# Optimization experiments

Hardware: AMD Instinct MI355X
Metric: run time of the kernel (lower is better)

The kernel has to match this reference:

```python
import jax, jax.numpy as jnp
import numpy as np

B, W, NN, EPG = 8, 16, 64, 1024   # batch, window, nodes/graph, trace-edges/graph
N = B * W * NN                     # 8192 flattened nodes
E = B * W * EPG                    # 131072 node-graph edges == trace rows
E2 = 4 * E                         # 524288 edge-graph (line-graph) edges
D_NODE = 128; D_LOG = 128; D_EDGE = 128
D_IN = D_NODE + D_LOG              # 256 = GATv2 node2node in_channels
H = 4
EPS = 1e-16                        # PyG softmax epsilon


def _lin(key, fan_in, fan_out):
    return jax.random.normal(key, (fan_in, fan_out), jnp.float32) * (1.0 / np.sqrt(fan_in))


def setup_inputs() -> dict:
    key = jax.random.key(0)
    ks = jax.random.split(key, 16)
    return {
        "x_node": jax.random.normal(ks[0], (B, W, NN, D_NODE), jnp.float32),
        "x_trace": jax.random.normal(ks[1], (B, W, EPG, D_EDGE), jnp.float32),
        "x_log": jax.random.normal(ks[2], (B, W, NN, D_LOG), jnp.float32),
        "node_adj": jax.random.randint(ks[3], (2, E), 0, N, jnp.int32),
        "edge_adj": jax.random.randint(ks[4], (2, E2), 0, E, jnp.int32),
        "edge_efea": jax.random.randint(ks[5], (E2,), 0, N, jnp.int32),
        # node2node GATv2Conv: in=256, heads=4, out/head=64, edge_dim=128
        "n2n_Wl": _lin(ks[6], D_IN, D_IN), "n2n_bl": jnp.zeros((D_IN,), jnp.float32),
        "n2n_Wr": _lin(ks[7], D_IN, D_IN), "n2n_br": jnp.zeros((D_IN,), jnp.float32),
        "n2n_We": _lin(ks[8], D_EDGE, D_IN),
        "n2n_att": jax.random.normal(ks[9], (H, D_IN // H), jnp.float32) * 0.1,
        "n2n_bias": jnp.zeros((D_IN,), jnp.float32),
        # egde2node GATv2Conv: in=128, heads=4, out/head=32, edge_dim=256
        "e2n_Wl": _lin(ks[10], D_EDGE, D_EDGE), "e2n_bl": jnp.zeros((D_EDGE,), jnp.float32),
        "e2n_Wr": _lin(ks[11], D_EDGE, D_EDGE), "e2n_br": jnp.zeros((D_EDGE,), jnp.float32),
        "e2n_We": _lin(ks[12], D_IN, D_EDGE),
        "e2n_att": jax.random.normal(ks[13], (H, D_EDGE // H), jnp.float32) * 0.1,
        "e2n_bias": jnp.zeros((D_EDGE,), jnp.float32),
    }


def gatv2(x, edge_index, edge_attr, Wl, bl, Wr, br, We, att, bias, num_nodes):
    """PyG GATv2Conv (eval mode, add_self_loops=False, concat heads)."""
    heads, C = att.shape
    src, dst = edge_index[0], edge_index[1]
    xl = (x @ Wl + bl).reshape(-1, heads, C)   # source transform [N,H,C]
    xr = (x @ Wr + br).reshape(-1, heads, C)   # target transform [N,H,C]
    e = (edge_attr @ We).reshape(-1, heads, C) # edge transform   [E,H,C]
    m = jax.nn.leaky_relu(xl[src] + xr[dst] + e, 0.2)  # [E,H,C]
    alpha = jnp.einsum('ehc,hc->eh', m, att)           # [E,H]
    amax = jax.ops.segment_max(alpha, dst, num_segments=num_nodes)
    ex = jnp.exp(alpha - amax[dst])
    denom = jax.ops.segment_sum(ex, dst, num_segments=num_nodes)
    a = ex / (denom[dst] + EPS)                        # per-target softmax
    out = jax.ops.segment_sum(a[:, :, None] * xl[src], dst, num_segments=num_nodes)
    return out.reshape(num_nodes, heads * C) + bias


def reference(x_node, x_trace, x_log, node_adj, edge_adj, edge_efea,
              n2n_Wl, n2n_bl, n2n_Wr, n2n_br, n2n_We, n2n_att, n2n_bias,
              e2n_Wl, e2n_bl, e2n_Wr, e2n_br, e2n_We, e2n_att, e2n_bias):
    node = jnp.concatenate([x_node, x_log], axis=-1).reshape(-1, D_IN)  # [N,256]
    trace = x_trace.reshape(-1, D_EDGE)                                 # [E,128]
    node = gatv2(node, node_adj, trace,
                 n2n_Wl, n2n_bl, n2n_Wr, n2n_br, n2n_We, n2n_att, n2n_bias, N)
    trace = gatv2(trace, edge_adj, node[edge_efea],
                  e2n_Wl, e2n_bl, e2n_Wr, e2n_br, e2n_We, e2n_att, e2n_bias, E)
    xn = node[:, :D_NODE].reshape(B, W, NN, D_NODE)
    xt = trace.reshape(B, W, EPG, D_EDGE)
    xlg = node[:, D_NODE:].reshape(B, W, NN, D_LOG)
    return (xn, xt, xlg)
```

## Files before the change

### kernel.cpp

```cpp
#include <hip/hip_runtime.h>
#include <hip/hip_bf16.h>

constexpr int N    = 8192;
constexpr int E    = 131072;
constexpr int E2   = 524288;

constexpr size_t XT_OFF  = (size_t)N * 128;
constexpr size_t XLG_OFF = XT_OFF + (size_t)E * 128;

typedef unsigned short u16;
typedef short s16x8 __attribute__((ext_vector_type(8)));
typedef float f32x4 __attribute__((ext_vector_type(4)));

__device__ __forceinline__ u16 f2bs(float f) {
    unsigned x = __float_as_uint(f);
    return (u16)((x + 0x7FFF + ((x >> 16) & 1)) >> 16);
}
__device__ __forceinline__ float bs2f(u16 u) {
    return __uint_as_float((unsigned)u << 16);
}

__global__ __launch_bounds__(256) void k_prep(
    const float* __restrict__ Wl, const float* __restrict__ Wr,
    const float* __restrict__ We, const float* __restrict__ Wl2,
    const float* __restrict__ Wr2, const float* __restrict__ We2,
    u16* __restrict__ Wlt, u16* __restrict__ Wrt, u16* __restrict__ Wet,
    u16* __restrict__ Wl2t, u16* __restrict__ Wr2t, u16* __restrict__ We2t)
{
    const int gid = blockIdx.x * 256 + threadIdx.x;
    const float* src; u16* dst; int base, Kk, sh, perm;
    if      (gid <  65536) { src = Wl;  dst = Wlt;  base = 0;      Kk = 256; sh = 8; perm = 0; }
    else if (gid < 131072) { src = Wr;  dst = Wrt;  base = 65536;  Kk = 256; sh = 8; perm = 0; }
    else if (gid < 163840) { src = We;  dst = Wet;  base = 131072; Kk = 128; sh = 8; perm = 1; }
    else if (gid < 180224) { src = Wl2; dst = Wl2t; base = 163840; Kk = 128; sh = 7; perm = 1; }
    else if (gid < 196608) { src = Wr2; dst = Wr2t; base = 180224; Kk = 128; sh = 7; perm = 1; }
    else                   { src = We2; dst = We2t; base = 196608; Kk = 256; sh = 7; perm = 0; }
    const int l = gid - base;
    const int k = l >> sh, nn = l & ((1 << sh) - 1);
    int ns = nn;
    if (perm) ns = (nn & ~63) | ((nn & 3) << 4) | ((nn >> 2) & 15);
    dst[(size_t)ns * Kk + k] = f2bs(src[l]);
}

__global__ void k_hist(const int* __restrict__ dst, int* __restrict__ cnt, int nE)
{
    int i = blockIdx.x * 256 + threadIdx.x;
    if (i < nE) atomicAdd(&cnt[dst[i]], 1);
}

__global__ __launch_bounds__(1024) void k_scan(
    const int* __restrict__ cnt, int* __restrict__ off, int* __restrict__ cur, int n)
{
    __shared__ int tile[8192];
    __shared__ int wsum[16];
    const int tid = threadIdx.x, lane = tid & 63, wv = tid >> 6;
    int carry = 0;
    for (int base = 0; base < n; base += 8192) {
        for (int i = tid; i < 8192; i += 1024) tile[i] = cnt[base + i];
        __syncthreads();
        const int st = tid * 8;
        int s = 0;
        for (int k = 0; k < 8; ++k) { int v = tile[st + k]; tile[st + k] = s; s += v; }
        const int tsum = s;
        int incl = s;
        for (int o = 1; o < 64; o <<= 1) {
            int v = __shfl_up(incl, o);
            if (lane >= o) incl += v;
        }
        if (lane == 63) wsum[wv] = incl;
        __syncthreads();
        int woff = 0;
        for (int wq = 0; wq < wv; ++wq) woff += wsum[wq];
        int tot = 0;
        for (int wq = 0; wq < 16; ++wq) tot += wsum[wq];
        const int add = carry + woff + incl - tsum;
        for (int k = 0; k < 8; ++k) {
            int o2 = add + tile[st + k];
            off[base + st + k] = o2;
            cur[base + st + k] = o2;
        }
        carry += tot;
        __syncthreads();
    }
    if (tid == 0) off[n] = carry;
}

__global__ void k_scatter1(const int* __restrict__ adj, int* __restrict__ cur,
                           int* __restrict__ srcc, int* __restrict__ pos1, int nE)
{
    int i = blockIdx.x * 256 + threadIdx.x;
    if (i < nE) {
        int pos = atomicAdd(&cur[adj[nE + i]], 1);
        srcc[pos] = adj[i];
        pos1[i] = pos;
    }
}

__global__ void k_scatter2(const int* __restrict__ eadj, const int* __restrict__ efea,
                           int* __restrict__ cur, int2* __restrict__ sf2, int nE)
{
    int i = blockIdx.x * 256 + threadIdx.x;
    if (i < nE) {
        int pos = atomicAdd(&cur[eadj[nE + i]], 1);
        sf2[pos] = make_int2(eadj[i], efea[i]);
    }
}

__global__ __launch_bounds__(256) void k_node_gemm(
    const float* __restrict__ x_node, const float* __restrict__ x_log,
    const u16* __restrict__ Wlt, const float* __restrict__ bl,
    const u16* __restrict__ Wrt, const float* __restrict__ br,
    u16* __restrict__ xl, u16* __restrict__ xr)
{
    __shared__ u16 A[32][260];
    const int n0 = blockIdx.x * 32;
    const int tid = threadIdx.x;
    for (int i = tid; i < 32 * 64; i += 256) {
        const int r = i >> 6, k4 = (i & 63) << 2;
        const float* srcp = (k4 < 128) ? &x_node[(size_t)(n0 + r) * 128 + k4]
                                       : &x_log [(size_t)(n0 + r) * 128 + (k4 - 128)];
        const float4 v = *(const float4*)srcp;
        ushort4 o; o.x = f2bs(v.x); o.y = f2bs(v.y); o.z = f2bs(v.z); o.w = f2bs(v.w);
        *(ushort4*)&A[r][k4] = o;
    }
    __syncthreads();
    const int w = tid >> 6, lane = tid & 63, lr = lane & 15, lq = lane >> 4;
    const u16* Wt     = (w < 2) ? Wlt : Wrt;
    const float* bias = (w < 2) ? bl : br;
    u16* outp         = (w < 2) ? xl : xr;
    const int cb = (w & 1) * 128;
    f32x4 acc[2][8] = {};
    for (int kb = 0; kb < 8; ++kb) {
        s16x8 afr0 = *(const s16x8*)&A[lr][kb * 32 + lq * 8];
        s16x8 afr1 = *(const s16x8*)&A[16 + lr][kb * 32 + lq * 8];
#pragma unroll
        for (int ct = 0; ct < 8; ++ct) {
            const int n = cb + ct * 16 + lr;
            s16x8 bfr = *(const s16x8*)&Wt[(size_t)n * 256 + kb * 32 + lq * 8];
            acc[0][ct] = __builtin_amdgcn_mfma_f32_16x16x32_bf16(afr0, bfr, acc[0][ct], 0, 0, 0);
            acc[1][ct] = __builtin_amdgcn_mfma_f32_16x16x32_bf16(afr1, bfr, acc[1][ct], 0, 0, 0);
        }
    }
#pragma unroll
    for (int rt = 0; rt < 2; ++rt)
#pragma unroll
        for (int ct = 0; ct < 8; ++ct) {
            const int col = cb + ct * 16 + lr;
            const float bv = bias[col];
#pragma unroll
            for (int reg = 0; reg < 4; ++reg) {
                const int row = n0 + rt * 16 + lq * 4 + reg;
                outp[(size_t)row * 256 + col] = f2bs(acc[rt][ct][reg] + bv);
            }
        }
}

constexpr int TPB_EDGE = 8;
__global__ __launch_bounds__(512) void k_edge_mm(
    const float* __restrict__ x_trace,
    const int* __restrict__ adj,
    const int* __restrict__ pos1,
    const u16* __restrict__ xl_n, const u16* __restrict__ xr_n,
    const u16* __restrict__ Wet,
    const u16* __restrict__ Wl2t, const float* __restrict__ bl2,
    const u16* __restrict__ Wr2t, const float* __restrict__ br2,
    const float* __restrict__ att,
    float* __restrict__ alpha, u16* __restrict__ xl_e, u16* __restrict__ xrst)
{
    __shared__ u16 A[2][32][132];
    __shared__ int ss[2][32], dd[2][32], pp[2][32];
    const int tid = threadIdx.x;
    const int w8 = tid >> 6;
    const int role = w8 >> 2;
    const int w = w8 & 3;
    const int lane = tid & 63, lr = lane & 15, lq = lane >> 4;

    s16x8 wf[4][4];
    const int cb2 = (w & 1) * 64;
    if (role == 0) {
#pragma unroll
        for (int kb = 0; kb < 4; ++kb)
#pragma unroll
            for (int ct = 0; ct < 4; ++ct)
                wf[kb][ct] = *(const s16x8*)&Wet[(size_t)(w * 64 + ct * 16 + lr) * 128 + kb * 32 + lq * 8];
    } else {
        const u16* Wt2 = (w < 2) ? Wl2t : Wr2t;
#pragma unroll
        for (int kb = 0; kb < 4; ++kb)
#pragma unroll
            for (int ct = 0; ct < 4; ++ct)
                wf[kb][ct] = *(const s16x8*)&Wt2[(size_t)(cb2 + ct * 16 + lr) * 128 + kb * 32 + lq * 8];
    }
    const float4 attq = *(const float4*)&att[w * 64 + lr * 4];
    const float4 b2q  = (role == 0) ? make_float4(0, 0, 0, 0)
        : *(const float4*)&((w < 2) ? bl2 : br2)[cb2 + lr * 4];

    const int tile0 = blockIdx.x * TPB_EDGE;
    {
        const int e0s = tile0 * 32;
        const int i0 = tid, i1 = tid + 512;
        {
            const int r = i0 >> 5, k4 = (i0 & 31) << 2;
            const float4 v = *(const float4*)&x_trace[(size_t)(e0s + r) * 128 + k4];
            ushort4 o; o.x = f2bs(v.x); o.y = f2bs(v.y); o.z = f2bs(v.z); o.w = f2bs(v.w);
            *(ushort4*)&A[0][r][k4] = o;
        }
        {
            const int r = i1 >> 5, k4 = (i1 & 31) << 2;
            const float4 v = *(const float4*)&x_trace[(size_t)(e0s + r) * 128 + k4];
            ushort4 o; o.x = f2bs(v.x); o.y = f2bs(v.y); o.z = f2bs(v.z); o.w = f2bs(v.w);
            *(ushort4*)&A[0][r][k4] = o;
        }
        if (tid < 32) {
            ss[0][tid] = adj[e0s + tid];
            dd[0][tid] = adj[E + e0s + tid];
            pp[0][tid] = pos1[e0s + tid];
        }
    }

    for (int t = 0; t < TPB_EDGE; ++t) {
        __syncthreads();
        const int b = t & 1;
        const int e0 = (tile0 + t) * 32;
        if (t + 1 < TPB_EDGE) {
            const int e0s = (tile0 + t + 1) * 32;
            const int bn = b ^ 1;
            {
                const int r = tid >> 5, k4 = (tid & 31) << 2;
                const float4 v = *(const float4*)&x_trace[(size_t)(e0s + r) * 128 + k4];
                ushort4 o; o.x = f2bs(v.x); o.y = f2bs(v.y); o.z = f2bs(v.z); o.w = f2bs(v.w);
                *(ushort4*)&A[bn][r][k4] = o;
            }
            {
                const int i1 = tid + 512;
                const int r = i1 >> 5, k4 = (i1 & 31) << 2;
                const float4 v = *(const float4*)&x_trace[(size_t)(e0s + r) * 128 + k4];
                ushort4 o; o.x = f2bs(v.x); o.y = f2bs(v.y); o.z = f2bs(v.z); o.w = f2bs(v.w);
                *(ushort4*)&A[bn][r][k4] = o;
            }
            if (tid < 32) {
                ss[bn][tid] = adj[e0s + tid];
                dd[bn][tid] = adj[E + e0s + tid];
                pp[bn][tid] = pos1[e0s + tid];
            }
        }

        if (role == 0) {
            const int co = w * 64 + lr * 4;
            ushort4 xlv[2][4], xrv[2][4];
#pragma unroll
            for (int rt = 0; rt < 2; ++rt)
#pragma unroll
                for (int reg = 0; reg < 4; ++reg) {
                    const int rowt = rt * 16 + lq * 4 + reg;
                    xlv[rt][reg] = *(const ushort4*)&xl_n[(size_t)ss[b][rowt] * 256 + co];
                    xrv[rt][reg] = *(const ushort4*)&xr_n[(size_t)dd[b][rowt] * 256 + co];
                }
            f32x4 acc1[2][4] = {};
#pragma unroll
            for (int kb = 0; kb < 4; ++kb) {
                s16x8 afr0 = *(const s16x8*)&A[b][lr][kb * 32 + lq * 8];
                s16x8 afr1 = *(const s16x8*)&A[b][16 + lr][kb * 32 + lq * 8];
#pragma unroll
                for (int ct = 0; ct < 4; ++ct) {
                    acc1[0][ct] = __builtin_amdgcn_mfma_f32_16x16x32_bf16(afr0, wf[kb][ct], acc1[0][ct], 0, 0, 0);
                    acc1[1][ct] = __builtin_amdgcn_mfma_f32_16x16x32_bf16(afr1, wf[kb][ct], acc1[1][ct], 0, 0, 0);
                }
            }
            float sums[2][4];
#pragma unroll
            for (int rt = 0; rt < 2; ++rt)
#pragma unroll
                for (int reg = 0; reg < 4; ++reg) {
                    float m0 = acc1[rt][0][reg] + bs2f(xlv[rt][reg].x) + bs2f(xrv[rt][reg].x);
                    float m1 = acc1[rt][1][reg] + bs2f(xlv[rt][reg].y) + bs2f(xrv[rt][reg].y);
                    float m2 = acc1[rt][2][reg] + bs2f(xlv[rt][reg].z) + bs2f(xrv[rt][reg].z);
                    float m3 = acc1[rt][3][reg] + bs2f(xlv[rt][reg].w) + bs2f(xrv[rt][reg].w);
                    m0 = m0 > 0.f ? m0 : 0.2f * m0;
                    m1 = m1 > 0.f ? m1 : 0.2f * m1;
                    m2 = m2 > 0.f ? m2 : 0.2f * m2;
                    m3 = m3 > 0.f ? m3 : 0.2f * m3;
                    sums[rt][reg] = m0 * attq.x + m1 * attq.y + m2 * attq.z + m3 * attq.w;
                }
#pragma unroll
            for (int rt = 0; rt < 2; ++rt)
#pragma unroll
                for (int reg = 0; reg < 4; ++reg) {
                    float p = sums[rt][reg];
                    p += __shfl_xor(p, 8);
                    p += __shfl_xor(p, 4);
                    p += __shfl_xor(p, 2);
                    p += __shfl_xor(p, 1);
                    if (lr == 0)
                        alpha[(size_t)pp[b][rt * 16 + lq * 4 + reg] * 4 + w] = p;
                }
        } else {
            f32x4 acc2[2][4] = {};
#pragma unroll
            for (int kb = 0; kb < 4; ++kb) {
                s16x8 afr0 = *(const s16x8*)&A[b][lr][kb * 32 + lq * 8];
                s16x8 afr1 = *(const s16x8*)&A[b][16 + lr][kb * 32 + lq * 8];
#pragma unroll
                for (int ct = 0; ct < 4; ++ct) {
                    acc2[0][ct] = __builtin_amdgcn_mfma_f32_16x16x32_bf16(afr0, wf[kb][ct], acc2[0][ct], 0, 0, 0);
                    acc2[1][ct] = __builtin_amdgcn_mfma_f32_16x16x32_bf16(afr1, wf[kb][ct], acc2[1][ct], 0, 0, 0);
                }
            }
#pragma unroll
            for (int rt = 0; rt < 2; ++rt)
#pragma unroll
                for (int reg = 0; reg < 4; ++reg) {
                    const int row = e0 + rt * 16 + lq * 4 + reg;
                    ushort4 o;
                    o.x = f2bs(acc2[rt][0][reg] + b2q.x);
                    o.y = f2bs(acc2[rt][1][reg] + b2q.y);
                    o.z = f2bs(acc2[rt][2][reg] + b2q.z);
                    o.w = f2bs(acc2[rt][3][reg] + b2q.w);
                    if (w < 2) *(ushort4*)&xl_e[(size_t)row * 128 + cb2 + lr * 4] = o;
                    else       *(ushort4*)&xrst[(size_t)row * 256 + cb2 + lr * 4] = o;
                }
        }
    }
}

__global__ __launch_bounds__(256) void k_fused1(
    const int* __restrict__ off, const int* __restrict__ srcc,
    const float* __restrict__ alphac,
    const u16* __restrict__ xl,
    const float* __restrict__ bias,
    float* __restrict__ out)
{
    const int wv = __builtin_amdgcn_readfirstlane(threadIdx.x >> 6);
    const int lane = threadIdx.x & 63;
    const int n = blockIdx.x * 4 + wv;
    const int c = lane * 4;
    const int h = lane >> 4;
    const int beg = off[n], end = off[n + 1];
    float mx = -INFINITY, den = 0.f;
    float a0 = 0.f, a1 = 0.f, a2 = 0.f, a3 = 0.f;
    int i = beg;
    while (i < end) {
        const int rem = end - i;
        int sa[8]; float pe[8];
#pragma unroll
        for (int k = 0; k < 8; ++k) {
            const int idx = i + (k < rem ? k : rem - 1);
            sa[k] = srcc[idx];
            pe[k] = alphac[(size_t)idx * 4 + h];
        }
        ushort4 xv[8];
#pragma unroll
        for (int k = 0; k < 8; ++k)
            xv[k] = *(const ushort4*)&xl[(size_t)sa[k] * 256 + c];
#pragma unroll
        for (int k = 0; k < 8; ++k) {
            const float p = (k < rem) ? pe[k] : -INFINITY;
            const float mnew = fmaxf(mx, p);
            const float sc = __expf(mx - mnew);
            const float ex = __expf(p - mnew);
            den = den * sc + ex;
            a0 = a0 * sc + ex * bs2f(xv[k].x);
            a1 = a1 * sc + ex * bs2f(xv[k].y);
            a2 = a2 * sc + ex * bs2f(xv[k].z);
            a3 = a3 * sc + ex * bs2f(xv[k].w);
            mx = mnew;
        }
        i += 8;
    }
    const float inv = 1.f / (den + 1e-16f);
    float4 r;
    r.x = a0 * inv + bias[c + 0];
    r.y = a1 * inv + bias[c + 1];
    r.z = a2 * inv + bias[c + 2];
    r.w = a3 * inv + bias[c + 3];
    if (lane < 32) *(float4*)&out[(size_t)n * 128 + c] = r;
    else           *(float4*)&out[XLG_OFF + (size_t)n * 128 + (c - 128)] = r;
}

__global__ __launch_bounds__(256) void k_proj_gemm(
    const float* __restrict__ out_node, const u16* __restrict__ We2t,
    u16* __restrict__ proj)
{
    __shared__ u16 A[32][260];
    const int n0 = blockIdx.x * 32;
    const int tid = threadIdx.x;
    for (int i = tid; i < 32 * 64; i += 256) {
        const int r = i >> 6, k4 = (i & 63) << 2;
        const float* srcp = (k4 < 128)
            ? &out_node[(size_t)(n0 + r) * 128 + k4]
            : &out_node[XLG_OFF + (size_t)(n0 + r) * 128 + (k4 - 128)];
        const float4 v = *(const float4*)srcp;
        ushort4 o; o.x = f2bs(v.x); o.y = f2bs(v.y); o.z = f2bs(v.z); o.w = f2bs(v.w);
        *(ushort4*)&A[r][k4] = o;
    }
    __syncthreads();
    const int w = tid >> 6, lane = tid & 63, lr = lane & 15, lq = lane >> 4;
    f32x4 acc[2][2] = {};
    for (int kb = 0; kb < 8; ++kb) {
        s16x8 afr0 = *(const s16x8*)&A[lr][kb * 32 + lq * 8];
        s16x8 afr1 = *(const s16x8*)&A[16 + lr][kb * 32 + lq * 8];
#pragma unroll
        for (int ct = 0; ct < 2; ++ct) {
            const int col = w * 32 + ct * 16 + lr;
            s16x8 bfr = *(const s16x8*)&We2t[(size_t)col * 256 + kb * 32 + lq * 8];
            acc[0][ct] = __builtin_amdgcn_mfma_f32_16x16x32_bf16(afr0, bfr, acc[0][ct], 0, 0, 0);
            acc[1][ct] = __builtin_amdgcn_mfma_f32_16x16x32_bf16(afr1, bfr, acc[1][ct], 0, 0, 0);
        }
    }
#pragma unroll
    for (int rt = 0; rt < 2; ++rt)
#pragma unroll
        for (int ct = 0; ct < 2; ++ct) {
            const int col = w * 32 + ct * 16 + lr;
#pragma unroll
            for (int reg = 0; reg < 4; ++reg) {
                const int row = n0 + rt * 16 + lq * 4 + reg;
                proj[(size_t)row * 128 + col] = f2bs(acc[rt][ct][reg]);
            }
        }
}

__global__ __launch_bounds__(256) void k_fused2(
    const int* __restrict__ off, const int2* __restrict__ sf2,
    const u16* __restrict__ xl,
    const u16* __restrict__ proj,
    const float* __restrict__ att,
    const float* __restrict__ bias,
    float* __restrict__ out)
{
    const int wv = __builtin_amdgcn_readfirstlane(threadIdx.x >> 6);
    const int lane = threadIdx.x & 63;
    const int d = blockIdx.x * 4 + wv;
    const int c = lane * 2;
    const u16* xrst = (const u16*)(out + XT_OFF);
    const unsigned xrp = *(const unsigned*)&xrst[(size_t)d * 256 + c];
    const float xr0 = bs2f((u16)(xrp & 0xffff));
    const float xr1 = bs2f((u16)(xrp >> 16));
    const float av0 = att[c], av1 = att[c + 1];
    const int beg = off[d], end = off[d + 1];
    float mx = -INFINITY, den = 0.f, a0 = 0.f, a1 = 0.f;
    int i = beg;
    while (i < end) {
        const int rem = end - i;
        int2 sf[4];
#pragma unroll
        for (int k = 0; k < 4; ++k) sf[k] = sf2[i + (k < rem ? k : rem - 1)];
        unsigned xv[4], pv[4];
#pragma unroll
        for (int k = 0; k < 4; ++k) {
            xv[k] = *(const unsigned*)&xl[(size_t)sf[k].x * 128 + c];
            pv[k] = *(const unsigned*)&proj[(size_t)sf[k].y * 128 + c];
        }
#pragma unroll
        for (int k = 0; k < 4; ++k) {
            const float x0 = bs2f((u16)(xv[k] & 0xffff));
            const float x1 = bs2f((u16)(xv[k] >> 16));
            float m0 = x0 + xr0 + bs2f((u16)(pv[k] & 0xffff));
            float m1 = x1 + xr1 + bs2f((u16)(pv[k] >> 16));
            m0 = m0 > 0.f ? m0 : 0.2f * m0;
            m1 = m1 > 0.f ? m1 : 0.2f * m1;
            float pp = m0 * av0 + m1 * av1;
            pp += __shfl_xor(pp, 8, 16);
            pp += __shfl_xor(pp, 4, 16);
            pp += __shfl_xor(pp, 2, 16);
            pp += __shfl_xor(pp, 1, 16);
            const float p = (k < rem) ? pp : -INFINITY;
            const float mnew = fmaxf(mx, p);
            const float sc = __expf(mx - mnew);
            const float ex = __expf(p - mnew);
            den = den * sc + ex;
            a0 = a0 * sc + ex * x0;
            a1 = a1 * sc + ex * x1;
            mx = mnew;
        }
        i += 4;
    }
    const float inv = 1.f / (den + 1e-16f);
    float2 o2;
    o2.x = a0 * inv + bias[c];
    o2.y = a1 * inv + bias[c + 1];
    *(float2*)&out[XT_OFF + (size_t)d * 128 + c] = o2;
}

extern "C" void kernel_launch(void* const* d_in, const int* in_sizes, int n_in,
                              void* d_out, int out_size, void* d_ws, size_t ws_size,
                              hipStream_t stream)
{
    const float* x_node   = (const float*)d_in[0];
    const float* x_trace  = (const float*)d_in[1];
    const float* x_log    = (const float*)d_in[2];
    const int*   node_adj = (const int*)d_in[3];
    const int*   edge_adj = (const int*)d_in[4];
    const int*   efea     = (const int*)d_in[5];
    const float* n2n_Wl   = (const float*)d_in[6];
    const float* n2n_bl   = (const float*)d_in[7];
    const float* n2n_Wr   = (const float*)d_in[8];
    const float* n2n_br   = (const float*)d_in[9];
    const float* n2n_We   = (const float*)d_in[10];
    const float* n2n_att  = (const float*)d_in[11];
    const float* n2n_bias = (const float*)d_in[12];
    const float* e2n_Wl   = (const float*)d_in[13];
    const float* e2n_bl   = (const float*)d_in[14];
    const float* e2n_Wr   = (const float*)d_in[15];
    const float* e2n_br   = (const float*)d_in[16];
    const float* e2n_We   = (const float*)d_in[17];
    const float* e2n_att  = (const float*)d_in[18];
    const float* e2n_bias = (const float*)d_in[19];
    float* out = (float*)d_out;

    char* w = (char*)d_ws;
    int*  cnt1   = (int*)w;   w += (size_t)N * 4;
    int*  cnt2   = (int*)w;   w += (size_t)E * 4;
    int*  off1   = (int*)w;   w += (size_t)(N + 4) * 4;
    int*  cur1   = (int*)w;   w += (size_t)N * 4;
    int*  src1   = (int*)w;   w += (size_t)E * 4;
    int*  pos1   = (int*)w;   w += (size_t)E * 4;
    float* alphac = (float*)w; w += (size_t)E * 4 * 4;
    int*  off2   = (int*)w;   w += (size_t)(E + 4) * 4;
    int*  cur2   = (int*)w;   w += (size_t)E * 4;
    int2* sf2    = (int2*)w;  w += (size_t)E2 * 8;
    u16*  xl_n   = (u16*)w;   w += (size_t)N * 256 * 2;
    u16*  xr_n   = (u16*)w;   w += (size_t)N * 256 * 2;
    u16*  xl_e   = (u16*)w;   w += (size_t)E * 128 * 2;
    u16*  proj   = (u16*)w;   w += (size_t)N * 128 * 2;
    u16*  Wlt    = (u16*)w;   w += (size_t)65536 * 2;
    u16*  Wrt    = (u16*)w;   w += (size_t)65536 * 2;
    u16*  Wet    = (u16*)w;   w += (size_t)32768 * 2;
    u16*  Wl2t   = (u16*)w;   w += (size_t)16384 * 2;
    u16*  Wr2t   = (u16*)w;   w += (size_t)16384 * 2;
    u16*  We2t   = (u16*)w;   w += (size_t)32768 * 2;

    hipMemsetAsync(d_ws, 0, (size_t)(N + E) * 4, stream);

    k_prep<<<896, 256, 0, stream>>>(n2n_Wl, n2n_Wr, n2n_We, e2n_Wl, e2n_Wr, e2n_We,
                                    Wlt, Wrt, Wet, Wl2t, Wr2t, We2t);
    k_hist<<<E / 256, 256, 0, stream>>>(node_adj + E, cnt1, E);
    k_scan<<<1, 1024, 0, stream>>>(cnt1, off1, cur1, N);
    k_scatter1<<<E / 256, 256, 0, stream>>>(node_adj, cur1, src1, pos1, E);
    k_hist<<<E2 / 256, 256, 0, stream>>>(edge_adj + E2, cnt2, E2);
    k_scan<<<1, 1024, 0, stream>>>(cnt2, off2, cur2, E);
    k_scatter2<<<E2 / 256, 256, 0, stream>>>(edge_adj, efea, cur2, sf2, E2);

    k_node_gemm<<<N / 32, 256, 0, stream>>>(x_node, x_log, Wlt, n2n_bl, Wrt, n2n_br,
                                            xl_n, xr_n);
    k_edge_mm<<<E / (32 * TPB_EDGE), 512, 0, stream>>>(x_trace, node_adj, pos1, xl_n, xr_n,
                                          Wet, Wl2t, e2n_bl, Wr2t, e2n_br,
                                          n2n_att, alphac, xl_e, (u16*)(out + XT_OFF));
    k_fused1<<<N / 4, 256, 0, stream>>>(off1, src1, alphac, xl_n, n2n_bias, out);

    k_proj_gemm<<<N / 32, 256, 0, stream>>>(out, We2t, proj);
    k_fused2<<<E / 4, 256, 0, stream>>>(off2, sf2, xl_e, proj,
                                        e2n_att, e2n_bias, out);
}
```

Before: 427.5 us.

## Merge CSR build kernels and parallelize scan across blocks; shrink edge tiles per block

Merges the two histogram passes and the two scatter passes into single launches covering both graphs. Replaces the single-block serial scan with a two-phase multi-block scan (per-tile partial scan, then carry add), so the E-sized scan runs across 16 blocks instead of looping in one. Also halves tiles per block in the edge matmul kernel to launch more blocks. This is meant to cut launch overhead and the serial scan bottleneck, at the cost of one extra launch per scan and more atomic contention mixing the two graphs.

New measurement: 400.4 us. -6.4%, faster.

```diff
diff --git a/kernel.cpp b/kernel.cpp
--- a/kernel.cpp
+++ b/kernel.cpp
@@ -42,67 +42,74 @@
     dst[(size_t)ns * Kk + k] = f2bs(src[l]);
 }
 
-__global__ void k_hist(const int* __restrict__ dst, int* __restrict__ cnt, int nE)
+__global__ void k_hist2(const int* __restrict__ d1, const int* __restrict__ d2,
+                        int* __restrict__ c1, int* __restrict__ c2)
 {
     int i = blockIdx.x * 256 + threadIdx.x;
-    if (i < nE) atomicAdd(&cnt[dst[i]], 1);
-}
-
-__global__ __launch_bounds__(1024) void k_scan(
-    const int* __restrict__ cnt, int* __restrict__ off, int* __restrict__ cur, int n)
+    if (i < E) atomicAdd(&c1[d1[i]], 1);
+    else { int j = i - E; atomicAdd(&c2[d2[j]], 1); }
+}
+
+__global__ __launch_bounds__(1024) void k_scan_part(
+    const int* __restrict__ cnt, int* __restrict__ off, int* __restrict__ tsums)
 {
     __shared__ int tile[8192];
     __shared__ int wsum[16];
     const int tid = threadIdx.x, lane = tid & 63, wv = tid >> 6;
+    const int base = blockIdx.x * 8192;
+    for (int i = tid; i < 8192; i += 1024) tile[i] = cnt[base + i];
+    __syncthreads();
+    const int st = tid * 8;
+    int s = 0;
+    for (int k = 0; k < 8; ++k) { int v = tile[st + k]; tile[st + k] = s; s += v; }
+    const int tsum = s;
+    int incl = s;
+    for (int o = 1; o < 64; o <<= 1) {
+        int v = __shfl_up(incl, o);
+        if (lane >= o) incl += v;
+    }
+    if (lane == 63) wsum[wv] = incl;
+    __syncthreads();
+    int woff = 0;
+    for (int wq = 0; wq < wv; ++wq) woff += wsum[wq];
+    const int add = woff + incl - tsum;
+    for (int k = 0; k < 8; ++k) off[base + st + k] = add + tile[st + k];
+    if (tid == 1023) tsums[blockIdx.x] = woff + incl;
+}
+
+__global__ __launch_bounds__(1024) void k_scan_add(
+    int* __restrict__ off, int* __restrict__ cur,
+    const int* __restrict__ tsums, int ntiles, int n)
+{
+    const int b = blockIdx.x;
     int carry = 0;
-    for (int base = 0; base < n; base += 8192) {
-        for (int i = tid; i < 8192; i += 1024) tile[i] = cnt[base + i];
-        __syncthreads();
-        const int st = tid * 8;
-        int s = 0;
-        for (int k = 0; k < 8; ++k) { int v = tile[st + k]; tile[st + k] = s; s += v; }
-        const int tsum = s;
-        int incl = s;
-        for (int o = 1; o < 64; o <<= 1) {
-            int v = __shfl_up(incl, o);
-            if (lane >= o) incl += v;
-        }
-        if (lane == 63) wsum[wv] = incl;
-        __syncthreads();
-        int woff = 0;
-        for (int wq = 0; wq < wv; ++wq) woff += wsum[wq];
-        int tot = 0;
-        for (int wq = 0; wq < 16; ++wq) tot += wsum[wq];
-        const int add = carry + woff + incl - tsum;
-        for (int k = 0; k < 8; ++k) {
-            int o2 = add + tile[st + k];
-            off[base + st + k] = o2;
-            cur[base + st + k] = o2;
-        }
-        carry += tot;
-        __syncthreads();
-    }
-    if (tid == 0) off[n] = carry;
-}
-
-__global__ void k_scatter1(const int* __restrict__ adj, int* __restrict__ cur,
-                           int* __restrict__ srcc, int* __restrict__ pos1, int nE)
+    for (int t = 0; t < b; ++t) carry += tsums[t];
+    const int base = b * 8192 + threadIdx.x * 8;
+#pragma unroll
+    for (int k = 0; k < 8; ++k) {
+        int v = off[base + k] + carry;
+        off[base + k] = v;
+        cur[base + k] = v;
+    }
+    if (b == ntiles - 1 && threadIdx.x == 1023)
+        off[n] = carry + tsums[b];
+}
+
+__global__ void k_scatterM(
+    const int* __restrict__ adj, int* __restrict__ cur1,
+    int* __restrict__ srcc, int* __restrict__ pos1,
+    const int* __restrict__ eadj, const int* __restrict__ efea,
+    int* __restrict__ cur2, int2* __restrict__ sf2)
 {
     int i = blockIdx.x * 256 + threadIdx.x;
-    if (i < nE) {
-        int pos = atomicAdd(&cur[adj[nE + i]], 1);
+    if (i < E) {
+        int pos = atomicAdd(&cur1[adj[E + i]], 1);
         srcc[pos] = adj[i];
         pos1[i] = pos;
-    }
-}
-
-__global__ void k_scatter2(const int* __restrict__ eadj, const int* __restrict__ efea,
-                           int* __restrict__ cur, int2* __restrict__ sf2, int nE)
-{
-    int i = blockIdx.x * 256 + threadIdx.x;
-    if (i < nE) {
-        int pos = atomicAdd(&cur[eadj[nE + i]], 1);
-        sf2[pos] = make_int2(eadj[i], efea[i]);
+    } else {
+        int j = i - E;
+        int pos = atomicAdd(&cur2[eadj[E2 + j]], 1);
+        sf2[pos] = make_int2(eadj[j], efea[j]);
     }
 }
 
@@ -155,7 +162,7 @@
         }
 }
 
-constexpr int TPB_EDGE = 8;
+constexpr int TPB_EDGE = 4;
 __global__ __launch_bounds__(512) void k_edge_mm(
     const float* __restrict__ x_trace,
     const int* __restrict__ adj,
@@ -529,17 +536,20 @@
     u16*  Wl2t   = (u16*)w;   w += (size_t)16384 * 2;
     u16*  Wr2t   = (u16*)w;   w += (size_t)16384 * 2;
     u16*  We2t   = (u16*)w;   w += (size_t)32768 * 2;
+    int*  tsum1  = (int*)w;   w += 64;
+    int*  tsum2  = (int*)w;   w += 64;
 
     hipMemsetAsync(d_ws, 0, (size_t)(N + E) * 4, stream);
 
     k_prep<<<896, 256, 0, stream>>>(n2n_Wl, n2n_Wr, n2n_We, e2n_Wl, e2n_Wr, e2n_We,
                                     Wlt, Wrt, Wet, Wl2t, Wr2t, We2t);
-    k_hist<<<E / 256, 256, 0, stream>>>(node_adj + E, cnt1, E);
-    k_scan<<<1, 1024, 0, stream>>>(cnt1, off1, cur1, N);
-    k_scatter1<<<E / 256, 256, 0, stream>>>(node_adj, cur1, src1, pos1, E);
-    k_hist<<<E2 / 256, 256, 0, stream>>>(edge_adj + E2, cnt2, E2);
-    k_scan<<<1, 1024, 0, stream>>>(cnt2, off2, cur2, E);
-    k_scatter2<<<E2 / 256, 256, 0, stream>>>(edge_adj, efea, cur2, sf2, E2);
+    k_hist2<<<(E + E2) / 256, 256, 0, stream>>>(node_adj + E, edge_adj + E2, cnt1, cnt2);
+    k_scan_part<<<N / 8192, 1024, 0, stream>>>(cnt1, off1, tsum1);
+    k_scan_part<<<E / 8192, 1024, 0, stream>>>(cnt2, off2, tsum2);
+    k_scan_add<<<N / 8192, 1024, 0, stream>>>(off1, cur1, tsum1, N / 8192, N);
+    k_scan_add<<<E / 8192, 1024, 0, stream>>>(off2, cur2, tsum2, E / 8192, E);
+    k_scatterM<<<(E + E2) / 256, 256, 0, stream>>>(node_adj, cur1, src1, pos1,
+                                                   edge_adj, efea, cur2, sf2);
 
     k_node_gemm<<<N / 32, 256, 0, stream>>>(x_node, x_log, Wlt, n2n_bl, Wrt, n2n_br,
                                             xl_n, xr_n);
```
